# Optimization experiments

Measured on AMD Instinct MI355X. Metric: run time of the kernel, lower is better.

The kernel has to match this reference:

```python
import jax, jax.numpy as jnp
import numpy as np

N = 50000      # nodes
E = 800000     # directed edges (before self loops)
IN = 64        # in_channels
HID = 96       # hidden_dim
HEADS = 4
C = HID // HEADS
L = 4          # num_layers
G = 1024       # num graphs (molecules)
OUT = 1
BN_EPS = 1e-5


def setup_inputs() -> dict:
    key = jax.random.key(0)
    ks = jax.random.split(key, 20)
    x = jax.random.normal(ks[0], (N, IN), jnp.float32)
    edge_index = jax.random.randint(ks[1], (2, E), 0, N, dtype=jnp.int32)
    batch = jnp.sort(jax.random.randint(ks[2], (N,), 0, G, dtype=jnp.int32))
    def lin(k, fi, fo):
        return jax.random.normal(k, (fi, fo), jnp.float32) / np.sqrt(fi)
    return {
        "x": x, "edge_index": edge_index, "batch": batch,
        "W_in": lin(ks[3], IN, HID), "b_in": jnp.zeros((HID,), jnp.float32),
        "Wg": jax.random.normal(ks[4], (L, HID, HID), jnp.float32) / np.sqrt(HID),
        "att_src": jax.random.normal(ks[5], (L, HEADS, C), jnp.float32) / np.sqrt(C),
        "att_dst": jax.random.normal(ks[6], (L, HEADS, C), jnp.float32) / np.sqrt(C),
        "bg": jnp.zeros((L, HID), jnp.float32),
        "gamma": jnp.ones((L, HID), jnp.float32),
        "beta": jnp.zeros((L, HID), jnp.float32),
        "rm": 0.1 * jax.random.normal(ks[7], (L, HID), jnp.float32),
        "rv": jax.random.uniform(ks[8], (L, HID), jnp.float32, 0.5, 1.5),
        "W_jk": lin(ks[9], HID * L, HID), "b_jk": jnp.zeros((HID,), jnp.float32),
        "W_h1": lin(ks[10], HID, HID), "b_h1": jnp.zeros((HID,), jnp.float32),
        "W_h2": lin(ks[11], HID, OUT), "b_h2": jnp.zeros((OUT,), jnp.float32),
    }


def gat_conv(h_in, src, dst, W, a_s, a_d, b):
    # PyG GATConv (concat=True, negative_slope=0.2), eval mode (no dropout)
    h = (h_in @ W).reshape(N, HEADS, C)                      # [N,H,C]
    e = (h * a_s).sum(-1)[src] + (h * a_d).sum(-1)[dst]      # [E',H]
    e = jax.nn.leaky_relu(e, 0.2)
    m = jax.ops.segment_max(e, dst, num_segments=N)          # segment softmax over dst
    p = jnp.exp(e - m[dst])
    z = jax.ops.segment_sum(p, dst, num_segments=N)
    alpha = p / (z[dst] + 1e-16)                             # [E',H]
    out = jax.ops.segment_sum(h[src] * alpha[:, :, None], dst, num_segments=N)
    return out.reshape(N, HID) + b


def reference(x, edge_index, batch, W_in, b_in, Wg, att_src, att_dst, bg,
              gamma, beta, rm, rv, W_jk, b_jk, W_h1, b_h1, W_h2, b_h2):
    # add self loops (PyG GATConv default)
    loops = jnp.arange(N, dtype=edge_index.dtype)
    src = jnp.concatenate([edge_index[0], loops])
    dst = jnp.concatenate([edge_index[1], loops])

    h = jax.nn.elu(x @ W_in + b_in)
    pooled = []
    for i in range(L):
        hn = gat_conv(h, src, dst, Wg[i], att_src[i], att_dst[i], bg[i])
        hn = (hn - rm[i]) / jnp.sqrt(rv[i] + BN_EPS) * gamma[i] + beta[i]
        h = h + jax.nn.elu(hn)                               # residual
        pooled.append(jax.ops.segment_sum(h, batch, num_segments=G))
    z = jax.nn.elu(jnp.concatenate(pooled, axis=-1) @ W_jk + b_jk)  # JK
    z = jax.nn.relu(z @ W_h1 + b_h1)
    return z @ W_h2 + b_h2                                    # [G, OUT]
```

## Files before the change

### kernel.cpp

```cpp
#include <hip/hip_runtime.h>
#include <hip/hip_bf16.h>
#include <math.h>

#define NODES 50000
#define EDGES 800000
#define EP    850000
#define INCH  64
#define HIDD  96
#define NHEAD 4
#define CHD   24
#define NLAY  4
#define NGRF  1024
#define BNEPS 1e-5f
#define NB    49

__device__ __forceinline__ float elu1(float v) { return v > 0.f ? v : __expf(v) - 1.f; }

__device__ __forceinline__ unsigned short f2bf(float f) {
    unsigned u = __float_as_uint(f);
    return (unsigned short)((u + 0x7fffu + ((u >> 16) & 1u)) >> 16);
}

__device__ __forceinline__ float rl_f(float v, int l) {
    return __int_as_float(__builtin_amdgcn_readlane(__float_as_int(v), l));
}

__device__ __forceinline__ float bnorm(float a, const float* __restrict__ bg,
                                       const float* __restrict__ rm, const float* __restrict__ rv,
                                       const float* __restrict__ gamma, const float* __restrict__ beta,
                                       int ch) {
    float hn = a + bg[ch];
    return (hn - rm[ch]) / sqrtf(rv[ch] + BNEPS) * gamma[ch] + beta[ch];
}

__device__ __forceinline__ void edge_sd(int e, const int* __restrict__ S,
                                        const int* __restrict__ D, int& s, int& d) {
    if (e < EDGES) { s = S[e]; d = D[e]; } else { s = e - EDGES; d = s; }
}


__global__ __launch_bounds__(256) void k_count(const int* __restrict__ S, const int* __restrict__ D,
                                               int* __restrict__ cnt) {
    int e = blockIdx.x * blockDim.x + threadIdx.x;
    if (e >= EP) return;
    int s, d; edge_sd(e, S, D, s, d);
    atomicAdd(&cnt[d], 1);
}

__global__ __launch_bounds__(1024) void k_scan1(const int* __restrict__ cnt,
                                                int* __restrict__ off, int* __restrict__ bsum) {
    __shared__ int sd[1024];
    int t = threadIdx.x;
    int i = blockIdx.x * 1024 + t;
    int v = (i < NODES) ? cnt[i] : 0;
    sd[t] = v; __syncthreads();
    for (int o = 1; o < 1024; o <<= 1) {
        int tv = (t >= o) ? sd[t - o] : 0;
        __syncthreads();
        sd[t] += tv; __syncthreads();
    }
    if (i < NODES) off[i] = sd[t] - v;
    if (t == 1023) bsum[blockIdx.x] = sd[1023];
}

__global__ __launch_bounds__(1024) void k_scan3m(int* __restrict__ off, const int* __restrict__ bsum,
                                                 int* __restrict__ cursor) {
    int carry = 0;
    for (int b = 0; b < blockIdx.x; ++b) carry += bsum[b];
    int i = blockIdx.x * 1024 + threadIdx.x;
    if (i < NODES) {
        int o = off[i] + carry;
        off[i] = o;
        cursor[i] = o;
    }
    if (i == 0) off[NODES] = EP;
}

__global__ __launch_bounds__(256) void k_scatter(const int* __restrict__ S, const int* __restrict__ D,
                                                 int* __restrict__ cursor, int* __restrict__ csr_src) {
    int e = blockIdx.x * blockDim.x + threadIdx.x;
    if (e >= EP) return;
    int s, d; edge_sd(e, S, D, s, d);
    int pos = atomicAdd(&cursor[d], 1);
    csr_src[pos] = s;
}


__global__ __launch_bounds__(256) void k_in_proj_proj(const float* __restrict__ x,
                                                      const float* __restrict__ W_in,
                                                      const float* __restrict__ b_in,
                                                      const float* __restrict__ Wg0,
                                                      const float* __restrict__ asrc,
                                                      const float* __restrict__ adst,
                                                      float* __restrict__ h,
                                                      unsigned* __restrict__ hpb,
                                                      float* __restrict__ as_,
                                                      float* __restrict__ ad_,
                                                      float* __restrict__ pooled_all) {
    __shared__ float Wl[HIDD * HIDD];
    int tid = threadIdx.x;
    for (size_t i = (size_t)blockIdx.x * 256 + tid; i < (size_t)NLAY * NGRF * HIDD;
         i += (size_t)gridDim.x * 256)
        pooled_all[i] = 0.f;
    for (int i = tid; i < INCH * HIDD / 4; i += 256)
        ((float4*)Wl)[i] = ((const float4*)W_in)[i];
    __syncthreads();

    int lane = tid & 63;
    int node = blockIdx.x * 64 + lane;
    bool valid = node < NODES;
    int head = tid >> 6;
    int cbase = head * CHD;

    {
        const float* __restrict__ xr = x + (size_t)node * INCH;
        float acc[CHD];
#pragma unroll
        for (int j = 0; j < CHD; ++j) acc[j] = b_in[cbase + j];
        if (valid) {
            for (int k0 = 0; k0 < INCH; k0 += 4) {
                float4 xv = *(const float4*)(xr + k0);
                const float xvv[4] = {xv.x, xv.y, xv.z, xv.w};
#pragma unroll
                for (int kk = 0; kk < 4; ++kk) {
#pragma unroll
                    for (int j4 = 0; j4 < CHD; j4 += 4) {
                        float4 wv = *(const float4*)(&Wl[(k0 + kk) * HIDD + cbase + j4]);
                        acc[j4 + 0] = fmaf(xvv[kk], wv.x, acc[j4 + 0]);
                        acc[j4 + 1] = fmaf(xvv[kk], wv.y, acc[j4 + 1]);
                        acc[j4 + 2] = fmaf(xvv[kk], wv.z, acc[j4 + 2]);
                        acc[j4 + 3] = fmaf(xvv[kk], wv.w, acc[j4 + 3]);
                    }
                }
            }
            float* hrow = h + (size_t)node * HIDD + cbase;
#pragma unroll
            for (int j = 0; j < CHD; ++j) hrow[j] = elu1(acc[j]);
        }
    }
    __syncthreads();
    for (int i = tid; i < HIDD * HIDD / 4; i += 256)
        ((float4*)Wl)[i] = ((const float4*)Wg0)[i];
    __syncthreads();

    const float* __restrict__ hr = h + (size_t)node * HIDD;
    float acc[CHD] = {};
    for (int k0 = 0; k0 < HIDD; k0 += 4) {
        float4 hv = *(const float4*)(hr + k0);
        const float hvv[4] = {hv.x, hv.y, hv.z, hv.w};
#pragma unroll
        for (int kk = 0; kk < 4; ++kk) {
#pragma unroll
            for (int j4 = 0; j4 < CHD; j4 += 4) {
                float4 wv = *(const float4*)(&Wl[(k0 + kk) * HIDD + cbase + j4]);
                acc[j4 + 0] = fmaf(hvv[kk], wv.x, acc[j4 + 0]);
                acc[j4 + 1] = fmaf(hvv[kk], wv.y, acc[j4 + 1]);
                acc[j4 + 2] = fmaf(hvv[kk], wv.z, acc[j4 + 2]);
                acc[j4 + 3] = fmaf(hvv[kk], wv.w, acc[j4 + 3]);
            }
        }
    }
    if (valid) {
        unsigned* orow = hpb + (size_t)node * (HIDD / 2) + cbase / 2;
#pragma unroll
        for (int j = 0; j < CHD; j += 2)
            orow[j / 2] = (unsigned)f2bf(acc[j]) | ((unsigned)f2bf(acc[j + 1]) << 16);
        const float* __restrict__ s = asrc + head * CHD;
        const float* __restrict__ d = adst + head * CHD;
        float sa = 0.f, da = 0.f;
#pragma unroll
        for (int j = 0; j < CHD; ++j) { sa = fmaf(acc[j], s[j], sa); da = fmaf(acc[j], d[j], da); }
        as_[node * NHEAD + head] = sa;
        ad_[node * NHEAD + head] = da;
    }
}


__global__ __launch_bounds__(256) void k_proj(const float* __restrict__ h,
                                              const float* __restrict__ W,
                                              const float* __restrict__ asrc,
                                              const float* __restrict__ adst,
                                              unsigned* __restrict__ hpb,
                                              float* __restrict__ as_,
                                              float* __restrict__ ad_) {
    __shared__ float Wl[HIDD * HIDD];
    int tid = threadIdx.x;
    for (int i = tid; i < HIDD * HIDD / 4; i += 256)
        ((float4*)Wl)[i] = ((const float4*)W)[i];
    __syncthreads();

    int node = blockIdx.x * 64 + (tid & 63);
    if (node >= NODES) return;
    int head = tid >> 6;
    int cbase = head * CHD;
    const float* __restrict__ hr = h + (size_t)node * HIDD;

    float acc[CHD] = {};
    for (int k0 = 0; k0 < HIDD; k0 += 4) {
        float4 hv = *(const float4*)(hr + k0);
        const float hvv[4] = {hv.x, hv.y, hv.z, hv.w};
#pragma unroll
        for (int kk = 0; kk < 4; ++kk) {
#pragma unroll
            for (int j4 = 0; j4 < CHD; j4 += 4) {
                float4 wv = *(const float4*)(&Wl[(k0 + kk) * HIDD + cbase + j4]);
                acc[j4 + 0] = fmaf(hvv[kk], wv.x, acc[j4 + 0]);
                acc[j4 + 1] = fmaf(hvv[kk], wv.y, acc[j4 + 1]);
                acc[j4 + 2] = fmaf(hvv[kk], wv.z, acc[j4 + 2]);
                acc[j4 + 3] = fmaf(hvv[kk], wv.w, acc[j4 + 3]);
            }
        }
    }
    unsigned* orow = hpb + (size_t)node * (HIDD / 2) + cbase / 2;
#pragma unroll
    for (int j = 0; j < CHD; j += 2)
        orow[j / 2] = (unsigned)f2bf(acc[j]) | ((unsigned)f2bf(acc[j + 1]) << 16);

    const float* __restrict__ s = asrc + head * CHD;
    const float* __restrict__ d = adst + head * CHD;
    float sa = 0.f, da = 0.f;
#pragma unroll
    for (int j = 0; j < CHD; ++j) { sa = fmaf(acc[j], s[j], sa); da = fmaf(acc[j], d[j], da); }
    as_[node * NHEAD + head] = sa;
    ad_[node * NHEAD + head] = da;
}


__global__ __launch_bounds__(256) void k_edge(const int* __restrict__ off,
                                              const int* __restrict__ csr,
                                              const float* __restrict__ as_,
                                              const float* __restrict__ ad_,
                                              const unsigned* __restrict__ hpb,
                                              const float* __restrict__ bg,
                                              const float* __restrict__ gamma,
                                              const float* __restrict__ beta,
                                              const float* __restrict__ rm,
                                              const float* __restrict__ rv,
                                              float* __restrict__ h,
                                              const int* __restrict__ batch,
                                              float* __restrict__ pooled) {
    __shared__ float plds[512];
    int tid = threadIdx.x;
    int lane = tid & 63;
    int n0 = __builtin_amdgcn_readfirstlane(blockIdx.x * 8 + (tid >> 6) * 2);
    int n1 = n0 + 1;
    int beg0 = off[n0], end0 = off[n0 + 1], end1 = off[n0 + 2];
    int beg1 = end0;

    int hd = lane & 3, slot = lane >> 2;
    float adv0 = ad_[n0 * NHEAD + hd];
    float adv1 = ad_[n1 * NHEAD + hd];
    const int hh = (lane < 48) ? (lane / 12) : 0;
    const bool gl = (lane < 48);
    const int wb = (tid & 192) * 2;

    float a00 = 0.f, a01 = 0.f, a10 = 0.f, a11 = 0.f, zA = 0.f, zB = 0.f;
    int ca = beg0, cb = beg1;
    while (ca < end0 || cb < end1) {
        int cntA = min(16, end0 - ca);
        int cntB = min(16, end1 - cb);
        int sA = 0, sB = 0;
        if (cntA > 0) {
            int i = ca + slot, ii = min(i, end0 - 1);
            sA = csr[ii];
            float ev = as_[sA * NHEAD + hd] + adv0;
            ev = ev > 0.f ? ev : 0.2f * ev;
            float p = (i < end0) ? __expf(ev) : 0.f;
            zA += p;
            plds[wb + lane] = p;
        }
        if (cntB > 0) {
            int i = cb + slot, ii = min(i, end1 - 1);
            sB = csr[ii];
            float ev = as_[sB * NHEAD + hd] + adv1;
            ev = ev > 0.f ? ev : 0.2f * ev;
            float p = (i < end1) ? __expf(ev) : 0.f;
            zB += p;
            plds[wb + 64 + lane] = p;
        }
        if (cntA > 0) {
#pragma unroll
            for (int j = 0; j < 16; ++j) {
                if (j < cntA) {
                    int sv = __builtin_amdgcn_readlane(sA, j * 4);
                    float al = plds[wb + j * 4 + hh];
                    if (gl) {
                        unsigned u = (hpb + (size_t)sv * (HIDD / 2))[lane];
                        a00 = fmaf(__uint_as_float(u << 16),         al, a00);
                        a01 = fmaf(__uint_as_float(u & 0xffff0000u), al, a01);
                    }
                }
            }
            ca += 16;
        }
        if (cntB > 0) {
#pragma unroll
            for (int j = 0; j < 16; ++j) {
                if (j < cntB) {
                    int sv = __builtin_amdgcn_readlane(sB, j * 4);
                    float al = plds[wb + 64 + j * 4 + hh];
                    if (gl) {
                        unsigned u = (hpb + (size_t)sv * (HIDD / 2))[lane];
                        a10 = fmaf(__uint_as_float(u << 16),         al, a10);
                        a11 = fmaf(__uint_as_float(u & 0xffff0000u), al, a11);
                    }
                }
            }
            cb += 16;
        }
    }
#pragma unroll
    for (int o = 4; o < 64; o <<= 1) { zA += __shfl_xor(zA, o); zB += __shfl_xor(zB, o); }
    float za0 = rl_f(zA, 0), za1 = rl_f(zA, 1), za2 = rl_f(zA, 2), za3 = rl_f(zA, 3);
    float zb0 = rl_f(zB, 0), zb1 = rl_f(zB, 1), zb2 = rl_f(zB, 2), zb3 = rl_f(zB, 3);
    float zAl = (hh & 1) ? za1 : za0, zAh = (hh & 1) ? za3 : za2;
    float zBl = (hh & 1) ? zb1 : zb0, zBh = (hh & 1) ? zb3 : zb2;
    float zhA = (hh & 2) ? zAh : zAl;
    float zhB = (hh & 2) ? zBh : zBl;

    int g0 = batch[n0], g1 = batch[n1];
    if (gl) {
        float izA = 1.f / zhA, izB = 1.f / zhB;
        a00 *= izA; a01 *= izA; a10 *= izB; a11 *= izB;
        int ch0 = 2 * lane, ch1 = ch0 + 1;
        float hn00 = bnorm(a00, bg, rm, rv, gamma, beta, ch0);
        float hn01 = bnorm(a01, bg, rm, rv, gamma, beta, ch1);
        float hn10 = bnorm(a10, bg, rm, rv, gamma, beta, ch0);
        float hn11 = bnorm(a11, bg, rm, rv, gamma, beta, ch1);
        float2 hv0 = *(float2*)(h + (size_t)n0 * HIDD + ch0);
        float2 hv1 = *(float2*)(h + (size_t)n1 * HIDD + ch0);
        hv0.x += elu1(hn00); hv0.y += elu1(hn01);
        hv1.x += elu1(hn10); hv1.y += elu1(hn11);
        *(float2*)(h + (size_t)n0 * HIDD + ch0) = hv0;
        *(float2*)(h + (size_t)n1 * HIDD + ch0) = hv1;
        if (g0 == g1) {
            atomicAdd(&pooled[g0 * HIDD + ch0], hv0.x + hv1.x);
            atomicAdd(&pooled[g0 * HIDD + ch1], hv0.y + hv1.y);
        } else {
            atomicAdd(&pooled[g0 * HIDD + ch0], hv0.x);
            atomicAdd(&pooled[g0 * HIDD + ch1], hv0.y);
            atomicAdd(&pooled[g1 * HIDD + ch0], hv1.x);
            atomicAdd(&pooled[g1 * HIDD + ch1], hv1.y);
        }
    }
}


__global__ __launch_bounds__(128) void k_head(const float* __restrict__ pooled,
                                              const float* __restrict__ Wjk, const float* __restrict__ bjk,
                                              const float* __restrict__ Wh1, const float* __restrict__ bh1,
                                              const float* __restrict__ Wh2, const float* __restrict__ bh2,
                                              float* __restrict__ out) {
    __shared__ float pin[NLAY * HIDD];
    __shared__ float z1[HIDD];
    __shared__ float z2[HIDD];
    int g = blockIdx.x, tid = threadIdx.x;
    for (int idx = tid; idx < NLAY * HIDD; idx += blockDim.x) {
        int l = idx / HIDD, c = idx % HIDD;
        pin[idx] = pooled[(size_t)l * NGRF * HIDD + (size_t)g * HIDD + c];
    }
    __syncthreads();
    for (int c = tid; c < HIDD; c += blockDim.x) {
        float a = bjk[c];
#pragma unroll 8
        for (int k = 0; k < NLAY * HIDD; ++k) a = fmaf(pin[k], Wjk[k * HIDD + c], a);
        z1[c] = elu1(a);
    }
    __syncthreads();
    for (int c = tid; c < HIDD; c += blockDim.x) {
        float a = bh1[c];
#pragma unroll 8
        for (int k = 0; k < HIDD; ++k) a = fmaf(z1[k], Wh1[k * HIDD + c], a);
        z2[c] = fmaxf(a, 0.f);
    }
    __syncthreads();
    if (tid < 64) {
        float a = 0.f;
        for (int k = tid; k < HIDD; k += 64) a = fmaf(z2[k], Wh2[k], a);
#pragma unroll
        for (int o = 32; o > 0; o >>= 1) a += __shfl_down(a, o);
        if (tid == 0) out[g] = a + bh2[0];
    }
}

extern "C" void kernel_launch(void* const* d_in, const int* in_sizes, int n_in,
                              void* d_out, int out_size, void* d_ws, size_t ws_size,
                              hipStream_t stream) {
    const float* x     = (const float*)d_in[0];
    const int*   ei    = (const int*)d_in[1];
    const int*   batch = (const int*)d_in[2];
    const float* W_in  = (const float*)d_in[3];
    const float* b_in  = (const float*)d_in[4];
    const float* Wg    = (const float*)d_in[5];
    const float* att_s = (const float*)d_in[6];
    const float* att_d = (const float*)d_in[7];
    const float* bg    = (const float*)d_in[8];
    const float* gamma = (const float*)d_in[9];
    const float* beta  = (const float*)d_in[10];
    const float* rm    = (const float*)d_in[11];
    const float* rv    = (const float*)d_in[12];
    const float* Wjk   = (const float*)d_in[13];
    const float* bjk   = (const float*)d_in[14];
    const float* Wh1   = (const float*)d_in[15];
    const float* bh1   = (const float*)d_in[16];
    const float* Wh2   = (const float*)d_in[17];
    const float* bh2   = (const float*)d_in[18];
    float* out = (float*)d_out;

    const int* S = ei;
    const int* Dd = ei + EDGES;

    float* ws = (float*)d_ws;
    float*    h      = ws;
    float*    as_    = h    + (size_t)NODES * HIDD;
    float*    ad_    = as_  + (size_t)NODES * NHEAD;
    float*    pooled = ad_  + (size_t)NODES * NHEAD;
    unsigned* hpb    = (unsigned*)(pooled + (size_t)NLAY * NGRF * HIDD);
    int*      off    = (int*)(hpb + (size_t)NODES * (HIDD / 2));
    int*      cursor = off    + NODES + 2;
    int*      csr    = cursor + NODES;
    int*      cnt    = csr    + EP;
    int*      bsum   = cnt    + NODES;

    hipMemsetAsync(cnt, 0, sizeof(int) * NODES, stream);

    const int TB = 256;
    int gE    = (EP + TB - 1) / TB;
    int gTile = (NODES + 63) / 64;
    int gEdge = NODES / 8;

    k_count<<<gE, TB, 0, stream>>>(S, Dd, cnt);
    k_scan1<<<NB, 1024, 0, stream>>>(cnt, off, bsum);
    k_scan3m<<<NB, 1024, 0, stream>>>(off, bsum, cursor);
    k_scatter<<<gE, TB, 0, stream>>>(S, Dd, cursor, csr);

    k_in_proj_proj<<<gTile, TB, 0, stream>>>(x, W_in, b_in, Wg, att_s, att_d,
                                             h, hpb, as_, ad_, pooled);
    k_edge<<<gEdge, TB, 0, stream>>>(off, csr, as_, ad_, hpb,
                                     bg, gamma, beta, rm, rv, h, batch, pooled);

    for (int i = 1; i < NLAY; ++i) {
        k_proj<<<gTile, TB, 0, stream>>>(h, Wg + (size_t)i * HIDD * HIDD,
                                         att_s + i * NHEAD * CHD, att_d + i * NHEAD * CHD,
                                         hpb, as_, ad_);
        k_edge<<<gEdge, TB, 0, stream>>>(off, csr, as_, ad_, hpb,
                                         bg + i * HIDD, gamma + i * HIDD, beta + i * HIDD,
                                         rm + i * HIDD, rv + i * HIDD, h, batch,
                                         pooled + (size_t)i * NGRF * HIDD);
    }

    k_head<<<NGRF, 128, 0, stream>>>(pooled, Wjk, bjk, Wh1, bh1, Wh2, bh2, out);
}
```

Measured before the change: 546.9 us.

## Fuse CSR build into one cooperative kernel and prefetch next edge chunk

Replaces the memset plus the count, two-pass scan and scatter kernels with a single cooperative kernel over 196 blocks, using grid-wide syncs between phases and a two-level block scan. This removes several launch gaps and the serial carry loop. The edge kernel also loads the next chunk's CSR source indices and attention scores before the current chunk's gather loop, to hide load latency. The cost is that the CSR build now runs on far fewer threads with grid-stride loops and pays for several grid barriers.

After: 619.5 us. +13.3%, slower.

```diff
diff --git a/kernel.cpp b/kernel.cpp
--- a/kernel.cpp
+++ b/kernel.cpp
@@ -1,6 +1,9 @@
 #include <hip/hip_runtime.h>
 #include <hip/hip_bf16.h>
+#include <hip/hip_cooperative_groups.h>
 #include <math.h>
+
+namespace cg = cooperative_groups;
 
 #define NODES 50000
 #define EDGES 800000
@@ -12,7 +15,7 @@
 #define NLAY  4
 #define NGRF  1024
 #define BNEPS 1e-5f
-#define NB    49
+#define CSRB  196
 
 __device__ __forceinline__ float elu1(float v) { return v > 0.f ? v : __expf(v) - 1.f; }
 
@@ -39,50 +42,58 @@
 }
 
 
-__global__ __launch_bounds__(256) void k_count(const int* __restrict__ S, const int* __restrict__ D,
-                                               int* __restrict__ cnt) {
-    int e = blockIdx.x * blockDim.x + threadIdx.x;
-    if (e >= EP) return;
-    int s, d; edge_sd(e, S, D, s, d);
-    atomicAdd(&cnt[d], 1);
-}
-
-__global__ __launch_bounds__(1024) void k_scan1(const int* __restrict__ cnt,
-                                                int* __restrict__ off, int* __restrict__ bsum) {
-    __shared__ int sd[1024];
+__global__ __launch_bounds__(256) void k_csr(const int* __restrict__ S, const int* __restrict__ D,
+                                             int* __restrict__ cnt, int* __restrict__ off,
+                                             int* __restrict__ cursor, int* __restrict__ csr,
+                                             int* __restrict__ bsum) {
+    cg::grid_group grid = cg::this_grid();
+    __shared__ int sd[256];
     int t = threadIdx.x;
-    int i = blockIdx.x * 1024 + t;
+    int gidx = blockIdx.x * 256 + t;
+    const int gsz = CSRB * 256;
+
+    for (int j = gidx; j < NODES; j += gsz) cnt[j] = 0;
+    grid.sync();
+    for (int e = gidx; e < EP; e += gsz) {
+        int s, d; edge_sd(e, S, D, s, d);
+        atomicAdd(&cnt[d], 1);
+    }
+    grid.sync();
+    int i = gidx;
     int v = (i < NODES) ? cnt[i] : 0;
     sd[t] = v; __syncthreads();
-    for (int o = 1; o < 1024; o <<= 1) {
+    for (int o = 1; o < 256; o <<= 1) {
         int tv = (t >= o) ? sd[t - o] : 0;
         __syncthreads();
         sd[t] += tv; __syncthreads();
     }
-    if (i < NODES) off[i] = sd[t] - v;
-    if (t == 1023) bsum[blockIdx.x] = sd[1023];
-}
-
-__global__ __launch_bounds__(1024) void k_scan3m(int* __restrict__ off, const int* __restrict__ bsum,
-                                                 int* __restrict__ cursor) {
-    int carry = 0;
-    for (int b = 0; b < blockIdx.x; ++b) carry += bsum[b];
-    int i = blockIdx.x * 1024 + threadIdx.x;
+    int excl = sd[t] - v;
+    if (t == 255) bsum[blockIdx.x] = sd[255];
+    grid.sync();
+    if (blockIdx.x == 0) {
+        int bv = (t < CSRB) ? bsum[t] : 0;
+        sd[t] = bv; __syncthreads();
+        for (int o = 1; o < 256; o <<= 1) {
+            int tv = (t >= o) ? sd[t - o] : 0;
+            __syncthreads();
+            sd[t] += tv; __syncthreads();
+        }
+        if (t < CSRB) bsum[t] = sd[t] - bv;
+    }
+    grid.sync();
+    int carry = bsum[blockIdx.x];
     if (i < NODES) {
-        int o = off[i] + carry;
+        int o = excl + carry;
         off[i] = o;
         cursor[i] = o;
     }
-    if (i == 0) off[NODES] = EP;
-}
-
-__global__ __launch_bounds__(256) void k_scatter(const int* __restrict__ S, const int* __restrict__ D,
-                                                 int* __restrict__ cursor, int* __restrict__ csr_src) {
-    int e = blockIdx.x * blockDim.x + threadIdx.x;
-    if (e >= EP) return;
-    int s, d; edge_sd(e, S, D, s, d);
-    int pos = atomicAdd(&cursor[d], 1);
-    csr_src[pos] = s;
+    if (gidx == 0) off[NODES] = EP;
+    grid.sync();
+    for (int e = gidx; e < EP; e += gsz) {
+        int s, d; edge_sd(e, S, D, s, d);
+        int pos = atomicAdd(&cursor[d], 1);
+        csr[pos] = s;
+    }
 }
 
 
@@ -256,28 +267,34 @@
 
     float a00 = 0.f, a01 = 0.f, a10 = 0.f, a11 = 0.f, zA = 0.f, zB = 0.f;
     int ca = beg0, cb = beg1;
+    int sA = 0, sB = 0;
+    float evA = 0.f, evB = 0.f;
+    if (ca < end0) { sA = csr[min(ca + slot, end0 - 1)]; evA = as_[sA * NHEAD + hd]; }
+    if (cb < end1) { sB = csr[min(cb + slot, end1 - 1)]; evB = as_[sB * NHEAD + hd]; }
+
     while (ca < end0 || cb < end1) {
         int cntA = min(16, end0 - ca);
         int cntB = min(16, end1 - cb);
-        int sA = 0, sB = 0;
         if (cntA > 0) {
-            int i = ca + slot, ii = min(i, end0 - 1);
-            sA = csr[ii];
-            float ev = as_[sA * NHEAD + hd] + adv0;
+            float ev = evA + adv0;
             ev = ev > 0.f ? ev : 0.2f * ev;
-            float p = (i < end0) ? __expf(ev) : 0.f;
+            float p = (ca + slot < end0) ? __expf(ev) : 0.f;
             zA += p;
             plds[wb + lane] = p;
         }
         if (cntB > 0) {
-            int i = cb + slot, ii = min(i, end1 - 1);
-            sB = csr[ii];
-            float ev = as_[sB * NHEAD + hd] + adv1;
+            float ev = evB + adv1;
             ev = ev > 0.f ? ev : 0.2f * ev;
-            float p = (i < end1) ? __expf(ev) : 0.f;
+            float p = (cb + slot < end1) ? __expf(ev) : 0.f;
             zB += p;
             plds[wb + 64 + lane] = p;
         }
+        int na = ca + (cntA > 0 ? 16 : 0);
+        int nb = cb + (cntB > 0 ? 16 : 0);
+        int sA2 = 0, sB2 = 0;
+        float evA2 = 0.f, evB2 = 0.f;
+        if (na < end0) { sA2 = csr[min(na + slot, end0 - 1)]; evA2 = as_[sA2 * NHEAD + hd]; }
+        if (nb < end1) { sB2 = csr[min(nb + slot, end1 - 1)]; evB2 = as_[sB2 * NHEAD + hd]; }
         if (cntA > 0) {
 #pragma unroll
             for (int j = 0; j < 16; ++j) {
@@ -291,7 +308,6 @@
                     }
                 }
             }
-            ca += 16;
         }
         if (cntB > 0) {
 #pragma unroll
@@ -306,8 +322,9 @@
                     }
                 }
             }
-            cb += 16;
-        }
+        }
+        ca = na; cb = nb;
+        sA = sA2; evA = evA2; sB = sB2; evB = evB2;
     }
 #pragma unroll
     for (int o = 4; o < 64; o <<= 1) { zA += __shfl_xor(zA, o); zB += __shfl_xor(zB, o); }
@@ -422,17 +439,15 @@
     int*      cnt    = csr    + EP;
     int*      bsum   = cnt    + NODES;
 
-    hipMemsetAsync(cnt, 0, sizeof(int) * NODES, stream);
-
     const int TB = 256;
-    int gE    = (EP + TB - 1) / TB;
     int gTile = (NODES + 63) / 64;
     int gEdge = NODES / 8;
 
-    k_count<<<gE, TB, 0, stream>>>(S, Dd, cnt);
-    k_scan1<<<NB, 1024, 0, stream>>>(cnt, off, bsum);
-    k_scan3m<<<NB, 1024, 0, stream>>>(off, bsum, cursor);
-    k_scatter<<<gE, TB, 0, stream>>>(S, Dd, cursor, csr);
+    {
+        void* args[] = {(void*)&S, (void*)&Dd, (void*)&cnt, (void*)&off,
+                        (void*)&cursor, (void*)&csr, (void*)&bsum};
+        hipLaunchCooperativeKernel((void*)k_csr, dim3(CSRB), dim3(TB), args, 0, stream);
+    }
 
     k_in_proj_proj<<<gTile, TB, 0, stream>>>(x, W_in, b_in, Wg, att_s, att_d,
                                              h, hpb, as_, ad_, pooled);
```
